# Optimization experiments

Hardware: AMD Instinct MI355X
Metric: run time of the kernel (lower is better)

## Reference

```python
import jax, jax.numpy as jnp
import numpy as np

N = 4096      # nodes = mi_num + dis_num
IN = 4096     # in_size = mi_num + dis_num
H = 1024      # hidd_list = [H, H]
P = 256       # num_proj_hidden
TAU = 0.5
ALPHA = 0.8


def setup_inputs() -> dict:
    key = jax.random.key(0)
    ks = jax.random.split(key, 24)
    u = lambda k, shape, s: jax.random.uniform(k, shape, jnp.float32, -s, s)
    sH = 1.0 / np.sqrt(H)      # HGNN_conv stdv = 1/sqrt(out_ft)
    sP2 = 1.0 / np.sqrt(2 * P)
    sP = 1.0 / np.sqrt(P)
    inp = {
        "x1": jax.random.normal(ks[0], (N, IN), jnp.float32),
        "adj1": jax.random.uniform(ks[1], (N, N), jnp.float32) / N,  # normalized dense hypergraph Laplacian
        "x2": jax.random.normal(ks[2], (N, IN), jnp.float32),
        "adj2": jax.random.uniform(ks[3], (N, N), jnp.float32) / N,
        # hgcn1 (view 1) layers
        "W1a": u(ks[4], (IN, H), sH), "b1a": u(ks[5], (H,), sH),
        "W1b": u(ks[6], (H, H), sH),  "b1b": u(ks[7], (H,), sH),
        # hgcn2 (view 2) layers
        "W2a": u(ks[8], (IN, H), sH), "b2a": u(ks[9], (H,), sH),
        "W2b": u(ks[10], (H, H), sH), "b2b": u(ks[11], (H,), sH),
        # shared projection head (Linear stored as [in, out])
        "fc1_w": u(ks[12], (2 * H, H), sH),     "fc1_b": u(ks[13], (H,), sH),
        "fc11_w": u(ks[14], (H, 2 * P), sP2),   "fc11_b": u(ks[15], (2 * P,), sP2),
        "fc12_w": u(ks[16], (2 * P, P), sP),    "fc12_b": u(ks[17], (P,), sP),
        "fc2_w": u(ks[18], (P, 2 * P), sP2),    "fc2_b": u(ks[19], (2 * P,), sP2),
        "fc3_w": u(ks[20], (2 * P, P), sP),     "fc3_b": u(ks[21], (P,), sP),
    }
    return inp


def _hgcn(x, G, Wa, ba, Wb, bb):
    # HGNN_conv: G @ (x @ W + b), then leaky_relu(0.25); JumpingKnowledge 'cat'
    h1 = jax.nn.leaky_relu(G @ (x @ Wa + ba), 0.25)   # [N, H]
    h2 = jax.nn.leaky_relu(G @ (h1 @ Wb + bb), 0.25)  # [N, H]
    return jnp.concatenate([h1, h2], axis=1)          # [N, 2H]


def _projection(z, fc1_w, fc1_b, fc11_w, fc11_b, fc12_w, fc12_b, fc2_w, fc2_b, fc3_w, fc3_b):
    e = jax.nn.elu
    z = e(z @ fc1_w + fc1_b)
    z = e(z @ fc11_w + fc11_b)
    z = e(z @ fc12_w + fc12_b)
    z = e(z @ fc2_w + fc2_b)
    return z @ fc3_w + fc3_b  # [N, P]


def _sim(z1, z2):
    # InfoNCE-style loss; F.normalize with eps 1e-12
    n1 = z1 / jnp.maximum(jnp.linalg.norm(z1, axis=1, keepdims=True), 1e-12)
    n2 = z2 / jnp.maximum(jnp.linalg.norm(z2, axis=1, keepdims=True), 1e-12)
    refl = jnp.exp((n1 @ n1.T) / TAU)      # [N, N]
    between = jnp.exp((n1 @ n2.T) / TAU)   # [N, N]
    d_b = jnp.diagonal(between)
    d_r = jnp.diagonal(refl)
    loss = -jnp.log(d_b / (refl.sum(1) + between.sum(1) - d_r))
    # torch: loss.sum(dim=-1).mean() on a 1-D vector == scalar sum
    return loss.sum()


def reference(x1, adj1, x2, adj2,
              W1a, b1a, W1b, b1b, W2a, b2a, W2b, b2b,
              fc1_w, fc1_b, fc11_w, fc11_b, fc12_w, fc12_b,
              fc2_w, fc2_b, fc3_w, fc3_b):
    z1 = _hgcn(x1, adj1, W1a, b1a, W1b, b1b)
    z2 = _hgcn(x2, adj2, W2a, b2a, W2b, b2b)
    proj = lambda z: _projection(z, fc1_w, fc1_b, fc11_w, fc11_b, fc12_w, fc12_b, fc2_w, fc2_b, fc3_w, fc3_b)
    h1 = proj(z1)
    h2 = proj(z2)
    loss = ALPHA * _sim(h1, h2) + (1.0 - ALPHA) * _sim(h2, h1)
    return (z1, z2, loss)
```

## Files before the change

kernel.cpp:

```cpp
#include <hip/hip_runtime.h>
#include <hip/hip_bf16.h>
#include <cstdint>

using bf16 = __hip_bfloat16;
typedef __attribute__((ext_vector_type(8))) short short8;
typedef __attribute__((ext_vector_type(4))) short short4v;
typedef __attribute__((ext_vector_type(4))) float floatx4;

#define DEVINL __device__ __forceinline__

DEVINL short bfbits(float v) { return __builtin_bit_cast(short, __float2bfloat16(v)); }

DEVINL void gload_lds16(const void* g, void* l) {
  __builtin_amdgcn_global_load_lds((const __attribute__((address_space(1))) void*)g,
                                   (__attribute__((address_space(3))) void*)l, 16, 0, 0);
}

template<int ACT> DEVINL float activate(float v) {
  if constexpr (ACT == 1) return v > 0.f ? v : 0.25f * v;
  else if constexpr (ACT == 2) return v > 0.f ? v : __expf(v) - 1.f;
  else return v;
}


template<int ACT, int TRANS, int BIAS, int AF32, int OF32, int DUAL>
__global__ __launch_bounds__(256, 2)
void gemm_bt(const void* __restrict__ A1, const void* __restrict__ A2, int lda,
             const bf16* __restrict__ B1, const bf16* __restrict__ B2, int ldb,
             const float* __restrict__ bias1, const float* __restrict__ bias2,
             void* __restrict__ out1, void* __restrict__ out2,
             bf16* __restrict__ outB1, bf16* __restrict__ outB2,
             int ldo, int K)
{
  const int gx = gridDim.x, gy = gridDim.y;
  const int nwg = gx * gy * gridDim.z;
  int bx, by, vz;
  if (nwg & 7) {
    bx = blockIdx.x; by = blockIdx.y; vz = blockIdx.z;
  } else {
    const int flat = blockIdx.x + gx * (blockIdx.y + gy * blockIdx.z);
    const int cpx = nwg >> 3;
    const int w = (flat & 7) * cpx + (flat >> 3);
    bx = w % gx;
    const int tmp = w / gx;
    by = tmp % gy;
    vz = tmp / gy;
  }

  const void* A = vz ? A2 : A1;
  const bf16* B = vz ? B2 : B1;
  const float* bias = vz ? bias2 : bias1;
  void* out = vz ? out2 : out1;
  bf16* outB = vz ? outB2 : outB1;

  constexpr int NBUF = AF32 ? 1 : 2;
  __shared__ bf16 At[NBUF][128 * 64];
  __shared__ bf16 Bt[NBUF][128 * 64];
  const int t = threadIdx.x;
  const int wave = t >> 6, lane = t & 63;
  const int mBase = by * 128, nBase = bx * 128;
  const int wm = (wave >> 1) * 64, wn = (wave & 1) * 64;
  const int q = lane >> 4, lm = lane & 15;
  const int rm = lm & 7;

  floatx4 acc[4][4];
#pragma unroll
  for (int i = 0; i < 4; i++)
#pragma unroll
    for (int j = 0; j < 4; j++) acc[i][j] = (floatx4){0.f, 0.f, 0.f, 0.f};

  if constexpr (!AF32) {
    auto STAGE = [&](int buf, int kb) {
#pragma unroll
      for (int i = 0; i < 4; i++) {
        const int c0 = i * 256 + wave * 64;
        const int c = c0 + lane;
        const int row = c >> 3;
        const int ls = (c & 7) ^ (row & 7);
        const bf16* ga = (const bf16*)A + (size_t)(mBase + row) * lda + kb + (ls << 3);
        const bf16* gb = B + (size_t)(nBase + row) * ldb + kb + (ls << 3);
        gload_lds16(ga, &At[buf][c0 * 8]);
        gload_lds16(gb, &Bt[buf][c0 * 8]);
      }
    };
    int cur = 0;
    STAGE(0, 0);
    for (int kb = 0; kb < K; kb += 64) {
      __syncthreads();
      if (kb + 64 < K) STAGE(cur ^ 1, kb + 64);
#pragma unroll
      for (int ks = 0; ks < 64; ks += 32) {
        const int sl = (ks >> 3) + q;
        short8 af[4], bfr[4];
#pragma unroll
        for (int i = 0; i < 4; i++)
          af[i] = *(const short8*)&At[cur][(wm + i * 16 + lm) * 64 + ((sl ^ rm) << 3)];
#pragma unroll
        for (int j = 0; j < 4; j++)
          bfr[j] = *(const short8*)&Bt[cur][(wn + j * 16 + lm) * 64 + ((sl ^ rm) << 3)];
#pragma unroll
        for (int i = 0; i < 4; i++)
#pragma unroll
          for (int j = 0; j < 4; j++)
            acc[i][j] = __builtin_amdgcn_mfma_f32_16x16x32_bf16(af[i], bfr[j], acc[i][j], 0, 0, 0);
      }
      cur ^= 1;
    }
  } else {
    floatx4 apl[4], aph[4];
    short8 bpb[4];
    auto LA = [&](int kb) {
#pragma unroll
      for (int i = 0; i < 4; i++) {
        int c = i * 256 + t;
        size_t off = (size_t)(mBase + (c >> 3)) * lda + kb + ((c & 7) << 3);
        const float* f = (const float*)A + off;
        apl[i] = *(const floatx4*)f;
        aph[i] = *(const floatx4*)(f + 4);
      }
    };
    auto LB = [&](int kb) {
#pragma unroll
      for (int i = 0; i < 4; i++) {
        int c = i * 256 + t;
        bpb[i] = *(const short8*)(B + (size_t)(nBase + (c >> 3)) * ldb + kb + ((c & 7) << 3));
      }
    };
    LA(0); LB(0);
    for (int kb = 0; kb < K; kb += 64) {
      __syncthreads();
#pragma unroll
      for (int i = 0; i < 4; i++) {
        int c = i * 256 + t;
        const int row = c >> 3;
        const int ps = (c & 7) ^ (row & 7);
        short8 r;
#pragma unroll
        for (int j = 0; j < 4; j++) { r[j] = bfbits(apl[i][j]); r[4 + j] = bfbits(aph[i][j]); }
        *(short8*)&At[0][row * 64 + (ps << 3)] = r;
        *(short8*)&Bt[0][row * 64 + (ps << 3)] = bpb[i];
      }
      __syncthreads();
      if (kb + 64 < K) { LA(kb + 64); LB(kb + 64); }
#pragma unroll
      for (int ks = 0; ks < 64; ks += 32) {
        const int sl = (ks >> 3) + q;
        short8 af[4], bfr[4];
#pragma unroll
        for (int i = 0; i < 4; i++)
          af[i] = *(const short8*)&At[0][(wm + i * 16 + lm) * 64 + ((sl ^ rm) << 3)];
#pragma unroll
        for (int j = 0; j < 4; j++)
          bfr[j] = *(const short8*)&Bt[0][(wn + j * 16 + lm) * 64 + ((sl ^ rm) << 3)];
#pragma unroll
        for (int i = 0; i < 4; i++)
#pragma unroll
          for (int j = 0; j < 4; j++)
            acc[i][j] = __builtin_amdgcn_mfma_f32_16x16x32_bf16(af[i], bfr[j], acc[i][j], 0, 0, 0);
      }
    }
  }

#pragma unroll
  for (int i = 0; i < 4; i++) {
#pragma unroll
    for (int j = 0; j < 4; j++) {
      const int col = nBase + wn + j * 16 + lm;
      float bv2 = 0.f;
      if constexpr (BIAS) bv2 = bias[col];
      if constexpr (TRANS) {
        short4v pk;
#pragma unroll
        for (int r = 0; r < 4; r++)
          pk[r] = bfbits(activate<ACT>(acc[i][j][r] + bv2));
        const int row = mBase + wm + i * 16 + q * 4;
        *(short4v*)&((bf16*)out)[(size_t)col * ldo + row] = pk;
      } else {
#pragma unroll
        for (int r = 0; r < 4; r++) {
          const int row = mBase + wm + i * 16 + q * 4 + r;
          float v = activate<ACT>(acc[i][j][r] + bv2);
          if constexpr (OF32) ((float*)out)[(size_t)row * ldo + col] = v;
          else ((bf16*)out)[(size_t)row * ldo + col] = __float2bfloat16(v);
          if constexpr (DUAL) outB[(size_t)row * ldo + col] = __float2bfloat16(v);
        }
      }
    }
  }
}

__global__ __launch_bounds__(256, 2)
void sim3(const bf16* __restrict__ n1, const bf16* __restrict__ n2,
          float* __restrict__ R11, float* __restrict__ R22,
          float* __restrict__ R12, float* __restrict__ C12)
{
  const bf16 *A, *B; float *Rs, *Cs;
  if (blockIdx.z == 0)      { A = n1; B = n1; Rs = R11; Cs = nullptr; }
  else if (blockIdx.z == 1) { A = n2; B = n2; Rs = R22; Cs = nullptr; }
  else                      { A = n1; B = n2; Rs = R12; Cs = C12; }

  __shared__ bf16 At[128 * 64];
  __shared__ bf16 Bt[128 * 64];
  const int t = threadIdx.x;
  const int wave = t >> 6, lane = t & 63;
  const int mBase = blockIdx.y * 128, nBase = blockIdx.x * 128;
  const int wm = (wave >> 1) * 64, wn = (wave & 1) * 64;
  const int q = lane >> 4, lm = lane & 15;
  const int rm = lm & 7;

  floatx4 acc[4][4];
#pragma unroll
  for (int i = 0; i < 4; i++)
#pragma unroll
    for (int j = 0; j < 4; j++) acc[i][j] = (floatx4){0.f, 0.f, 0.f, 0.f};

  short8 apb[4], bpb[4];
  auto LD = [&](int kb) {
#pragma unroll
    for (int i = 0; i < 4; i++) {
      int c = i * 256 + t;
      apb[i] = *(const short8*)(A + (size_t)(mBase + (c >> 3)) * 256 + kb + ((c & 7) << 3));
      bpb[i] = *(const short8*)(B + (size_t)(nBase + (c >> 3)) * 256 + kb + ((c & 7) << 3));
    }
  };

  LD(0);
  for (int kb = 0; kb < 256; kb += 64) {
    __syncthreads();
#pragma unroll
    for (int i = 0; i < 4; i++) {
      int c = i * 256 + t;
      const int row = c >> 3;
      const int ps = (c & 7) ^ (row & 7);
      *(short8*)&At[row * 64 + (ps << 3)] = apb[i];
      *(short8*)&Bt[row * 64 + (ps << 3)] = bpb[i];
    }
    __syncthreads();
    if (kb + 64 < 256) LD(kb + 64);
#pragma unroll
    for (int ks = 0; ks < 64; ks += 32) {
      const int sl = (ks >> 3) + q;
      short8 af[4], bfr[4];
#pragma unroll
      for (int i = 0; i < 4; i++)
        af[i] = *(const short8*)&At[(wm + i * 16 + lm) * 64 + ((sl ^ rm) << 3)];
#pragma unroll
      for (int j = 0; j < 4; j++)
        bfr[j] = *(const short8*)&Bt[(wn + j * 16 + lm) * 64 + ((sl ^ rm) << 3)];
#pragma unroll
      for (int i = 0; i < 4; i++)
#pragma unroll
        for (int j = 0; j < 4; j++)
          acc[i][j] = __builtin_amdgcn_mfma_f32_16x16x32_bf16(af[i], bfr[j], acc[i][j], 0, 0, 0);
    }
  }

  float rs[4][4], cs[4];
#pragma unroll
  for (int i = 0; i < 4; i++) { cs[i] = 0.f;
#pragma unroll
    for (int r = 0; r < 4; r++) rs[i][r] = 0.f; }

#pragma unroll
  for (int i = 0; i < 4; i++)
#pragma unroll
    for (int j = 0; j < 4; j++)
#pragma unroll
      for (int r = 0; r < 4; r++) {
        float e = __expf(2.f * acc[i][j][r]);
        rs[i][r] += e;
        cs[j] += e;
      }

#pragma unroll
  for (int i = 0; i < 4; i++)
#pragma unroll
    for (int r = 0; r < 4; r++) {
      float v = rs[i][r];
      v += __shfl_xor(v, 1); v += __shfl_xor(v, 2);
      v += __shfl_xor(v, 4); v += __shfl_xor(v, 8);
      if (lm == 0) atomicAdd(&Rs[mBase + wm + i * 16 + q * 4 + r], v);
    }
  if (Cs) {
#pragma unroll
    for (int j = 0; j < 4; j++) {
      float v = cs[j];
      v += __shfl_xor(v, 16); v += __shfl_xor(v, 32);
      if (lane < 16) atomicAdd(&Cs[nBase + wn + j * 16 + lane], v);
    }
  }
}

__global__ void transpose2_f32_bf16(const float* __restrict__ in1, const float* __restrict__ in2,
                                    bf16* __restrict__ out1, bf16* __restrict__ out2, int R, int C)
{
  const float* in = blockIdx.z ? in2 : in1;
  bf16* out = blockIdx.z ? out2 : out1;
  __shared__ float tile[32][33];
  const int bx = blockIdx.x * 32;
  const int by = blockIdx.y * 32;
  const int tx = threadIdx.x & 31, ty = threadIdx.x >> 5;
#pragma unroll
  for (int s = 0; s < 4; s++) {
    int r = ty + s * 8;
    tile[r][tx] = in[(size_t)(by + r) * C + bx + tx];
  }
  __syncthreads();
#pragma unroll
  for (int s = 0; s < 4; s++) {
    int r = ty + s * 8;
    out[(size_t)(bx + r) * R + by + tx] = __float2bfloat16(tile[tx][r]);
  }
}

__global__ void convert2_f32_bf16(const float* __restrict__ in1, const float* __restrict__ in2,
                                  bf16* __restrict__ out1, bf16* __restrict__ out2, int n8)
{
  const float* in = blockIdx.z ? in2 : in1;
  bf16* out = blockIdx.z ? out2 : out1;
  const int i = blockIdx.x * 256 + threadIdx.x;
  if (i >= n8) return;
  const size_t off = (size_t)i * 8;
  floatx4 a = *(const floatx4*)(in + off);
  floatx4 b = *(const floatx4*)(in + off + 4);
  short8 r;
#pragma unroll
  for (int j = 0; j < 4; j++) { r[j] = bfbits(a[j]); r[4 + j] = bfbits(b[j]); }
  *(short8*)(out + off) = r;
}

__global__ void zero_f32(float* __restrict__ p, int n)
{
  int i = blockIdx.x * blockDim.x + threadIdx.x;
  if (i < n) p[i] = 0.f;
}

__global__ void norm_rows2(const bf16* __restrict__ h1, const bf16* __restrict__ h2,
                           bf16* __restrict__ o1, bf16* __restrict__ o2)
{
  const bf16* h = blockIdx.z ? h2 : h1;
  bf16* o = blockIdx.z ? o2 : o1;
  const int row = blockIdx.x * 4 + (threadIdx.x >> 6);
  const int lane = threadIdx.x & 63;
  float v[4]; float ss = 0.f;
#pragma unroll
  for (int j = 0; j < 4; j++) {
    v[j] = __bfloat162float(h[(size_t)row * 256 + lane * 4 + j]);
    ss += v[j] * v[j];
  }
  for (int m = 1; m < 64; m <<= 1) ss += __shfl_xor(ss, m);
  const float s = 1.0f / fmaxf(sqrtf(ss), 1e-12f);
#pragma unroll
  for (int j = 0; j < 4; j++)
    o[(size_t)row * 256 + lane * 4 + j] = __float2bfloat16(v[j] * s);
}

__global__ void loss_partial(const bf16* __restrict__ n1, const bf16* __restrict__ n2,
                             const float* __restrict__ R11, const float* __restrict__ R12,
                             const float* __restrict__ R22, const float* __restrict__ C12,
                             float* __restrict__ lossAcc)
{
  const int row = blockIdx.x * 4 + (threadIdx.x >> 6);
  const int lane = threadIdx.x & 63;
  float d12 = 0.f, d11 = 0.f, d22 = 0.f;
#pragma unroll
  for (int j = 0; j < 4; j++) {
    float a = __bfloat162float(n1[(size_t)row * 256 + lane * 4 + j]);
    float b = __bfloat162float(n2[(size_t)row * 256 + lane * 4 + j]);
    d12 += a * b; d11 += a * a; d22 += b * b;
  }
  for (int m = 1; m < 64; m <<= 1) {
    d12 += __shfl_xor(d12, m); d11 += __shfl_xor(d11, m); d22 += __shfl_xor(d22, m);
  }
  if (lane == 0) {
    float a1 = fmaxf(R11[row] + R12[row] - __expf(2.f * d11), 1e-20f);
    float a2 = fmaxf(R22[row] + C12[row] - __expf(2.f * d22), 1e-20f);
    float l1 = logf(a1) - 2.f * d12;
    float l2 = logf(a2) - 2.f * d12;
    atomicAdd(lossAcc, 0.8f * l1 + 0.2f * l2);
  }
}

__global__ void finalize_loss(const float* __restrict__ lossAcc, float* __restrict__ out)
{
  if (threadIdx.x == 0) out[0] = *lossAcc;
}

extern "C" void kernel_launch(void* const* d_in, const int* in_sizes, int n_in,
                              void* d_out, int out_size, void* d_ws, size_t ws_size,
                              hipStream_t stream)
{
  (void)in_sizes; (void)n_in; (void)out_size;
  const float* x1   = (const float*)d_in[0];
  const float* adj1 = (const float*)d_in[1];
  const float* x2   = (const float*)d_in[2];
  const float* adj2 = (const float*)d_in[3];
  const float* W1a  = (const float*)d_in[4];  const float* b1a = (const float*)d_in[5];
  const float* W1b  = (const float*)d_in[6];  const float* b1b = (const float*)d_in[7];
  const float* W2a  = (const float*)d_in[8];  const float* b2a = (const float*)d_in[9];
  const float* W2b  = (const float*)d_in[10]; const float* b2b = (const float*)d_in[11];
  const float* fc1w = (const float*)d_in[12]; const float* fc1b = (const float*)d_in[13];
  const float* fc11w= (const float*)d_in[14]; const float* fc11b= (const float*)d_in[15];
  const float* fc12w= (const float*)d_in[16]; const float* fc12b= (const float*)d_in[17];
  const float* fc2w = (const float*)d_in[18]; const float* fc2b = (const float*)d_in[19];
  const float* fc3w = (const float*)d_in[20]; const float* fc3b = (const float*)d_in[21];

  float* z1 = (float*)d_out;
  float* z2 = z1 + (size_t)4096 * 2048;
  float* lossOut = z1 + (size_t)2 * 4096 * 2048;

  const size_t MB = 1u << 20;
  char* w = (char*)d_ws;
  bf16* WT1  = (bf16*)(w);
  bf16* WT2  = (bf16*)(w + 8 * MB);
  bf16* TT1  = (bf16*)(w + 16 * MB);
  bf16* TT2  = (bf16*)(w + 24 * MB);
  bf16* zB1  = (bf16*)(w + 32 * MB);
  bf16* zB2  = (bf16*)(w + 48 * MB);
  bf16* fc1T = (bf16*)(w + 64 * MB);
  bf16* fc11T= (bf16*)(w + 68 * MB);
  bf16* fc12T= (bf16*)(w + 69 * MB);
  bf16* fc2T = (bf16*)(w + 69 * MB + 256 * 1024);
  bf16* fc3T = (bf16*)(w + 69 * MB + 512 * 1024);
  float* R11 = (float*)(w + 69 * MB + 768 * 1024);
  float* R12 = R11 + 4096;
  float* R22 = R12 + 4096;
  float* C12 = R22 + 4096;
  float* lossAcc = C12 + 4096;
  bf16* P1_1 = (bf16*)(w);
  bf16* P1_2 = (bf16*)(w + 8 * MB);
  bf16* P2_1 = (bf16*)(w + 16 * MB);
  bf16* P2_2 = (bf16*)(w + 20 * MB);
  bf16* P3_1 = (bf16*)(w + 24 * MB);
  bf16* P3_2 = (bf16*)(w + 26 * MB);
  bf16* P4_1 = (bf16*)(w + 28 * MB);
  bf16* P4_2 = (bf16*)(w);
  bf16* Hp1  = (bf16*)(w + 4 * MB);
  bf16* Hp2  = (bf16*)(w + 6 * MB);
  bf16* n1   = (bf16*)(w + 8 * MB);
  bf16* n2   = (bf16*)(w + 10 * MB);
  bf16* adjB1 = (bf16*)(w + 72 * MB);
  bf16* adjB2 = (bf16*)(w + 104 * MB);
  bf16* xB1   = (bf16*)(w + 136 * MB);
  bf16* xB2   = (bf16*)(w + 168 * MB);
  const bool cvtAdj = ws_size >= 136 * MB;
  const bool cvtX   = ws_size >= 200 * MB;

  dim3 blk(256);

  zero_f32<<<dim3(65), blk, 0, stream>>>(R11, 4 * 4096 + 1);

  if (cvtAdj)
    convert2_f32_bf16<<<dim3(8192, 1, 2), blk, 0, stream>>>(adj1, adj2, adjB1, adjB2, 2097152);
  if (cvtX)
    convert2_f32_bf16<<<dim3(8192, 1, 2), blk, 0, stream>>>(x1, x2, xB1, xB2, 2097152);

  transpose2_f32_bf16<<<dim3(32, 64, 1), blk, 0, stream>>>(fc1w, fc1w, fc1T, fc1T, 2048, 1024);
  transpose2_f32_bf16<<<dim3(16, 32, 1), blk, 0, stream>>>(fc11w, fc11w, fc11T, fc11T, 1024, 512);
  transpose2_f32_bf16<<<dim3(8, 16, 1),  blk, 0, stream>>>(fc12w, fc12w, fc12T, fc12T, 512, 256);
  transpose2_f32_bf16<<<dim3(16, 8, 1),  blk, 0, stream>>>(fc2w, fc2w, fc2T, fc2T, 256, 512);
  transpose2_f32_bf16<<<dim3(8, 16, 1),  blk, 0, stream>>>(fc3w, fc3w, fc3T, fc3T, 512, 256);

  transpose2_f32_bf16<<<dim3(32, 128, 2), blk, 0, stream>>>(W1a, W2a, WT1, WT2, 4096, 1024);
  if (cvtX)
    gemm_bt<0, 1, 1, 0, 0, 0><<<dim3(8, 32, 2), blk, 0, stream>>>(
        xB1, xB2, 4096, WT1, WT2, 4096, b1a, b2a, TT1, TT2, nullptr, nullptr, 4096, 4096);
  else
    gemm_bt<0, 1, 1, 1, 0, 0><<<dim3(8, 32, 2), blk, 0, stream>>>(
        x1, x2, 4096, WT1, WT2, 4096, b1a, b2a, TT1, TT2, nullptr, nullptr, 4096, 4096);
  if (cvtAdj)
    gemm_bt<1, 0, 0, 0, 1, 1><<<dim3(8, 32, 2), blk, 0, stream>>>(
        adjB1, adjB2, 4096, TT1, TT2, 4096, nullptr, nullptr, z1, z2, zB1, zB2, 2048, 4096);
  else
    gemm_bt<1, 0, 0, 1, 1, 1><<<dim3(8, 32, 2), blk, 0, stream>>>(
        adj1, adj2, 4096, TT1, TT2, 4096, nullptr, nullptr, z1, z2, zB1, zB2, 2048, 4096);
  transpose2_f32_bf16<<<dim3(32, 32, 2), blk, 0, stream>>>(W1b, W2b, WT1, WT2, 1024, 1024);
  gemm_bt<0, 1, 1, 0, 0, 0><<<dim3(8, 32, 2), blk, 0, stream>>>(
      zB1, zB2, 2048, WT1, WT2, 1024, b1b, b2b, TT1, TT2, nullptr, nullptr, 4096, 1024);
  if (cvtAdj)
    gemm_bt<1, 0, 0, 0, 1, 1><<<dim3(8, 32, 2), blk, 0, stream>>>(
        adjB1, adjB2, 4096, TT1, TT2, 4096, nullptr, nullptr, z1 + 1024, z2 + 1024, zB1 + 1024, zB2 + 1024, 2048, 4096);
  else
    gemm_bt<1, 0, 0, 1, 1, 1><<<dim3(8, 32, 2), blk, 0, stream>>>(
        adj1, adj2, 4096, TT1, TT2, 4096, nullptr, nullptr, z1 + 1024, z2 + 1024, zB1 + 1024, zB2 + 1024, 2048, 4096);

  gemm_bt<2, 0, 1, 0, 0, 0><<<dim3(8, 32, 2), blk, 0, stream>>>(
      zB1, zB2, 2048, fc1T, fc1T, 2048, fc1b, fc1b, P1_1, P1_2, nullptr, nullptr, 1024, 2048);
  gemm_bt<2, 0, 1, 0, 0, 0><<<dim3(4, 32, 2), blk, 0, stream>>>(
      P1_1, P1_2, 1024, fc11T, fc11T, 1024, fc11b, fc11b, P2_1, P2_2, nullptr, nullptr, 512, 1024);
  gemm_bt<2, 0, 1, 0, 0, 0><<<dim3(2, 32, 2), blk, 0, stream>>>(
      P2_1, P2_2, 512, fc12T, fc12T, 512, fc12b, fc12b, P3_1, P3_2, nullptr, nullptr, 256, 512);
  gemm_bt<2, 0, 1, 0, 0, 0><<<dim3(4, 32, 2), blk, 0, stream>>>(
      P3_1, P3_2, 256, fc2T, fc2T, 256, fc2b, fc2b, P4_1, P4_2, nullptr, nullptr, 512, 256);
  gemm_bt<0, 0, 1, 0, 0, 0><<<dim3(2, 32, 2), blk, 0, stream>>>(
      P4_1, P4_2, 512, fc3T, fc3T, 512, fc3b, fc3b, Hp1, Hp2, nullptr, nullptr, 256, 512);
  norm_rows2<<<dim3(1024, 1, 2), blk, 0, stream>>>(Hp1, Hp2, n1, n2);

  sim3<<<dim3(32, 32, 3), blk, 0, stream>>>(n1, n2, R11, R22, R12, C12);

  loss_partial<<<dim3(1024), blk, 0, stream>>>(n1, n2, R11, R12, R22, C12, lossAcc);
  finalize_loss<<<dim3(1), dim3(64), 0, stream>>>(lossAcc, lossOut);
}
```

Measured before the change: 830.9 us.

## Load B operand fragments directly from global into registers, drop B LDS tile

B tiles are no longer staged through shared memory. Each wave loads its own B MFMA fragments straight from global memory into registers, software-pipelined across the two k-substeps. Dropping the B LDS buffer halves shared memory use, and the launch bound rises to 3 blocks per SM. The tile swizzle order is also flipped so that row tiles vary fastest. This trades LDS traffic and syncs for redundant, less-coalesced global loads of B: each B fragment is read by the two waves that share wn.

```diff
diff --git a/kernel.cpp b/kernel.cpp
--- a/kernel.cpp
+++ b/kernel.cpp
@@ -22,9 +22,8 @@
   else return v;
 }
 
-
 template<int ACT, int TRANS, int BIAS, int AF32, int OF32, int DUAL>
-__global__ __launch_bounds__(256, 2)
+__global__ __launch_bounds__(256, 3)
 void gemm_bt(const void* __restrict__ A1, const void* __restrict__ A2, int lda,
              const bf16* __restrict__ B1, const bf16* __restrict__ B2, int ldb,
              const float* __restrict__ bias1, const float* __restrict__ bias2,
@@ -41,10 +40,10 @@
     const int flat = blockIdx.x + gx * (blockIdx.y + gy * blockIdx.z);
     const int cpx = nwg >> 3;
     const int w = (flat & 7) * cpx + (flat >> 3);
-    bx = w % gx;
-    const int tmp = w / gx;
-    by = tmp % gy;
-    vz = tmp / gy;
+    by = w % gy;
+    const int tmp = w / gy;
+    bx = tmp % gx;
+    vz = tmp / gx;
   }
 
   const void* A = vz ? A2 : A1;
@@ -55,7 +54,6 @@
 
   constexpr int NBUF = AF32 ? 1 : 2;
   __shared__ bf16 At[NBUF][128 * 64];
-  __shared__ bf16 Bt[NBUF][128 * 64];
   const int t = threadIdx.x;
   const int wave = t >> 6, lane = t & 63;
   const int mBase = by * 128, nBase = bx * 128;
@@ -69,6 +67,26 @@
 #pragma unroll
     for (int j = 0; j < 4; j++) acc[i][j] = (floatx4){0.f, 0.f, 0.f, 0.f};
 
+  auto LBF = [&](short8 (&dst)[4], int kb, int ks) {
+#pragma unroll
+    for (int j = 0; j < 4; j++)
+      dst[j] = *(const short8*)(B + (size_t)(nBase + wn + j * 16 + lm) * ldb + kb + ks + q * 8);
+  };
+  auto LDA = [&](short8 (&af)[4], int buf, int sl) {
+#pragma unroll
+    for (int i = 0; i < 4; i++)
+      af[i] = *(const short8*)&At[buf][(wm + i * 16 + lm) * 64 + (((sl + q) ^ rm) << 3)];
+  };
+  auto MM = [&](short8 (&af)[4], short8 (&b)[4]) {
+#pragma unroll
+    for (int i = 0; i < 4; i++)
+#pragma unroll
+      for (int j = 0; j < 4; j++)
+        acc[i][j] = __builtin_amdgcn_mfma_f32_16x16x32_bf16(af[i], b[j], acc[i][j], 0, 0, 0);
+  };
+
+  short8 bC[4], bN[4];
+
   if constexpr (!AF32) {
     auto STAGE = [&](int buf, int kb) {
 #pragma unroll
@@ -78,37 +96,28 @@
         const int row = c >> 3;
         const int ls = (c & 7) ^ (row & 7);
         const bf16* ga = (const bf16*)A + (size_t)(mBase + row) * lda + kb + (ls << 3);
-        const bf16* gb = B + (size_t)(nBase + row) * ldb + kb + (ls << 3);
         gload_lds16(ga, &At[buf][c0 * 8]);
-        gload_lds16(gb, &Bt[buf][c0 * 8]);
       }
     };
     int cur = 0;
     STAGE(0, 0);
+    LBF(bC, 0, 0);
     for (int kb = 0; kb < K; kb += 64) {
       __syncthreads();
-      if (kb + 64 < K) STAGE(cur ^ 1, kb + 64);
-#pragma unroll
-      for (int ks = 0; ks < 64; ks += 32) {
-        const int sl = (ks >> 3) + q;
-        short8 af[4], bfr[4];
-#pragma unroll
-        for (int i = 0; i < 4; i++)
-          af[i] = *(const short8*)&At[cur][(wm + i * 16 + lm) * 64 + ((sl ^ rm) << 3)];
-#pragma unroll
-        for (int j = 0; j < 4; j++)
-          bfr[j] = *(const short8*)&Bt[cur][(wn + j * 16 + lm) * 64 + ((sl ^ rm) << 3)];
-#pragma unroll
-        for (int i = 0; i < 4; i++)
-#pragma unroll
-          for (int j = 0; j < 4; j++)
-            acc[i][j] = __builtin_amdgcn_mfma_f32_16x16x32_bf16(af[i], bfr[j], acc[i][j], 0, 0, 0);
-      }
+      const bool more = (kb + 64 < K);
+      if (more) STAGE(cur ^ 1, kb + 64);
+      LBF(bN, kb, 32);
+      short8 af[4];
+      LDA(af, cur, 0);
+      MM(af, bC);
+      if (more) LBF(bC, kb + 64, 0);
+      short8 ag[4];
+      LDA(ag, cur, 4);
+      MM(ag, bN);
       cur ^= 1;
     }
   } else {
     floatx4 apl[4], aph[4];
-    short8 bpb[4];
     auto LA = [&](int kb) {
 #pragma unroll
       for (int i = 0; i < 4; i++) {
@@ -119,14 +128,8 @@
         aph[i] = *(const floatx4*)(f + 4);
       }
     };
-    auto LB = [&](int kb) {
-#pragma unroll
-      for (int i = 0; i < 4; i++) {
-        int c = i * 256 + t;
-        bpb[i] = *(const short8*)(B + (size_t)(nBase + (c >> 3)) * ldb + kb + ((c & 7) << 3));
-      }
-    };
-    LA(0); LB(0);
+    LA(0);
+    LBF(bC, 0, 0);
     for (int kb = 0; kb < K; kb += 64) {
       __syncthreads();
 #pragma unroll
@@ -138,26 +141,18 @@
 #pragma unroll
         for (int j = 0; j < 4; j++) { r[j] = bfbits(apl[i][j]); r[4 + j] = bfbits(aph[i][j]); }
         *(short8*)&At[0][row * 64 + (ps << 3)] = r;
-        *(short8*)&Bt[0][row * 64 + (ps << 3)] = bpb[i];
       }
       __syncthreads();
-      if (kb + 64 < K) { LA(kb + 64); LB(kb + 64); }
-#pragma unroll
-      for (int ks = 0; ks < 64; ks += 32) {
-        const int sl = (ks >> 3) + q;
-        short8 af[4], bfr[4];
-#pragma unroll
-        for (int i = 0; i < 4; i++)
-          af[i] = *(const short8*)&At[0][(wm + i * 16 + lm) * 64 + ((sl ^ rm) << 3)];
-#pragma unroll
-        for (int j = 0; j < 4; j++)
-          bfr[j] = *(const short8*)&Bt[0][(wn + j * 16 + lm) * 64 + ((sl ^ rm) << 3)];
-#pragma unroll
-        for (int i = 0; i < 4; i++)
-#pragma unroll
-          for (int j = 0; j < 4; j++)
-            acc[i][j] = __builtin_amdgcn_mfma_f32_16x16x32_bf16(af[i], bfr[j], acc[i][j], 0, 0, 0);
-      }
+      const bool more = (kb + 64 < K);
+      if (more) LA(kb + 64);
+      LBF(bN, kb, 32);
+      short8 af[4];
+      LDA(af, 0, 0);
+      MM(af, bC);
+      if (more) LBF(bC, kb + 64, 0);
+      short8 ag[4];
+      LDA(ag, 0, 4);
+      MM(ag, bN);
     }
   }
 
```

Result: slower. 1.071 ms (+28.8%).

## Shrink GEMM tile to 128x64 and load sim3 operands directly from global

Applied to the files above, without the earlier changes.

The generic GEMM tile goes from 128x128 to 128x64, with half-size B staging and a 4x2 accumulator per wave. Launch bounds rise to 3 blocks per SM and every grid's x dimension is doubled to match. The sim3 kernel drops its LDS staging and reads MFMA fragments straight from global memory, relying on cache for the small K=256 operands. Smaller tiles raise occupancy and parallelism but cut arithmetic intensity per loaded byte, and the uncoalesced direct global fragment loads in sim3 may cost bandwidth.

```diff
diff --git a/kernel.cpp b/kernel.cpp
--- a/kernel.cpp
+++ b/kernel.cpp
@@ -22,9 +22,8 @@
   else return v;
 }
 
-
 template<int ACT, int TRANS, int BIAS, int AF32, int OF32, int DUAL>
-__global__ __launch_bounds__(256, 2)
+__global__ __launch_bounds__(256, 3)
 void gemm_bt(const void* __restrict__ A1, const void* __restrict__ A2, int lda,
              const bf16* __restrict__ B1, const bf16* __restrict__ B2, int ldb,
              const float* __restrict__ bias1, const float* __restrict__ bias2,
@@ -55,19 +54,37 @@
 
   constexpr int NBUF = AF32 ? 1 : 2;
   __shared__ bf16 At[NBUF][128 * 64];
-  __shared__ bf16 Bt[NBUF][128 * 64];
+  __shared__ bf16 Bt[NBUF][64 * 64];
   const int t = threadIdx.x;
   const int wave = t >> 6, lane = t & 63;
-  const int mBase = by * 128, nBase = bx * 128;
-  const int wm = (wave >> 1) * 64, wn = (wave & 1) * 64;
+  const int mBase = by * 128, nBase = bx * 64;
+  const int wm = (wave >> 1) * 64, wn = (wave & 1) * 32;
   const int q = lane >> 4, lm = lane & 15;
   const int rm = lm & 7;
 
-  floatx4 acc[4][4];
+  floatx4 acc[4][2];
 #pragma unroll
   for (int i = 0; i < 4; i++)
 #pragma unroll
-    for (int j = 0; j < 4; j++) acc[i][j] = (floatx4){0.f, 0.f, 0.f, 0.f};
+    for (int j = 0; j < 2; j++) acc[i][j] = (floatx4){0.f, 0.f, 0.f, 0.f};
+
+  auto LDA = [&](short8 (&af)[4], int buf, int sl) {
+#pragma unroll
+    for (int i = 0; i < 4; i++)
+      af[i] = *(const short8*)&At[buf][(wm + i * 16 + lm) * 64 + (((sl + q) ^ rm) << 3)];
+  };
+  auto LDB = [&](short8 (&bfr)[2], int buf, int sl) {
+#pragma unroll
+    for (int j = 0; j < 2; j++)
+      bfr[j] = *(const short8*)&Bt[buf][(wn + j * 16 + lm) * 64 + (((sl + q) ^ rm) << 3)];
+  };
+  auto MM = [&](short8 (&af)[4], short8 (&bfr)[2]) {
+#pragma unroll
+    for (int i = 0; i < 4; i++)
+#pragma unroll
+      for (int j = 0; j < 2; j++)
+        acc[i][j] = __builtin_amdgcn_mfma_f32_16x16x32_bf16(af[i], bfr[j], acc[i][j], 0, 0, 0);
+  };
 
   if constexpr (!AF32) {
     auto STAGE = [&](int buf, int kb) {
@@ -77,10 +94,17 @@
         const int c = c0 + lane;
         const int row = c >> 3;
         const int ls = (c & 7) ^ (row & 7);
-        const bf16* ga = (const bf16*)A + (size_t)(mBase + row) * lda + kb + (ls << 3);
-        const bf16* gb = B + (size_t)(nBase + row) * ldb + kb + (ls << 3);
-        gload_lds16(ga, &At[buf][c0 * 8]);
-        gload_lds16(gb, &Bt[buf][c0 * 8]);
+        gload_lds16((const bf16*)A + (size_t)(mBase + row) * lda + kb + (ls << 3),
+                    &At[buf][c0 * 8]);
+      }
+#pragma unroll
+      for (int i = 0; i < 2; i++) {
+        const int c0 = i * 256 + wave * 64;
+        const int c = c0 + lane;
+        const int row = c >> 3;
+        const int ls = (c & 7) ^ (row & 7);
+        gload_lds16(B + (size_t)(nBase + row) * ldb + kb + (ls << 3),
+                    &Bt[buf][c0 * 8]);
       }
     };
     int cur = 0;
@@ -88,40 +112,28 @@
     for (int kb = 0; kb < K; kb += 64) {
       __syncthreads();
       if (kb + 64 < K) STAGE(cur ^ 1, kb + 64);
-#pragma unroll
-      for (int ks = 0; ks < 64; ks += 32) {
-        const int sl = (ks >> 3) + q;
-        short8 af[4], bfr[4];
-#pragma unroll
-        for (int i = 0; i < 4; i++)
-          af[i] = *(const short8*)&At[cur][(wm + i * 16 + lm) * 64 + ((sl ^ rm) << 3)];
-#pragma unroll
-        for (int j = 0; j < 4; j++)
-          bfr[j] = *(const short8*)&Bt[cur][(wn + j * 16 + lm) * 64 + ((sl ^ rm) << 3)];
-#pragma unroll
-        for (int i = 0; i < 4; i++)
-#pragma unroll
-          for (int j = 0; j < 4; j++)
-            acc[i][j] = __builtin_amdgcn_mfma_f32_16x16x32_bf16(af[i], bfr[j], acc[i][j], 0, 0, 0);
-      }
+      short8 af[4], bfr[2];
+      LDA(af, cur, 0); LDB(bfr, cur, 0);
+      MM(af, bfr);
+      LDA(af, cur, 4); LDB(bfr, cur, 4);
+      MM(af, bfr);
       cur ^= 1;
     }
   } else {
     floatx4 apl[4], aph[4];
-    short8 bpb[4];
+    short8 bpb[2];
     auto LA = [&](int kb) {
 #pragma unroll
       for (int i = 0; i < 4; i++) {
         int c = i * 256 + t;
-        size_t off = (size_t)(mBase + (c >> 3)) * lda + kb + ((c & 7) << 3);
-        const float* f = (const float*)A + off;
+        const float* f = (const float*)A + (size_t)(mBase + (c >> 3)) * lda + kb + ((c & 7) << 3);
         apl[i] = *(const floatx4*)f;
         aph[i] = *(const floatx4*)(f + 4);
       }
     };
     auto LB = [&](int kb) {
 #pragma unroll
-      for (int i = 0; i < 4; i++) {
+      for (int i = 0; i < 2; i++) {
         int c = i * 256 + t;
         bpb[i] = *(const short8*)(B + (size_t)(nBase + (c >> 3)) * ldb + kb + ((c & 7) << 3));
       }
@@ -138,33 +150,28 @@
 #pragma unroll
         for (int j = 0; j < 4; j++) { r[j] = bfbits(apl[i][j]); r[4 + j] = bfbits(aph[i][j]); }
         *(short8*)&At[0][row * 64 + (ps << 3)] = r;
+      }
+#pragma unroll
+      for (int i = 0; i < 2; i++) {
+        int c = i * 256 + t;
+        const int row = c >> 3;
+        const int ps = (c & 7) ^ (row & 7);
         *(short8*)&Bt[0][row * 64 + (ps << 3)] = bpb[i];
       }
       __syncthreads();
       if (kb + 64 < K) { LA(kb + 64); LB(kb + 64); }
-#pragma unroll
-      for (int ks = 0; ks < 64; ks += 32) {
-        const int sl = (ks >> 3) + q;
-        short8 af[4], bfr[4];
-#pragma unroll
-        for (int i = 0; i < 4; i++)
-          af[i] = *(const short8*)&At[0][(wm + i * 16 + lm) * 64 + ((sl ^ rm) << 3)];
-#pragma unroll
-        for (int j = 0; j < 4; j++)
-          bfr[j] = *(const short8*)&Bt[0][(wn + j * 16 + lm) * 64 + ((sl ^ rm) << 3)];
-#pragma unroll
-        for (int i = 0; i < 4; i++)
-#pragma unroll
-          for (int j = 0; j < 4; j++)
-            acc[i][j] = __builtin_amdgcn_mfma_f32_16x16x32_bf16(af[i], bfr[j], acc[i][j], 0, 0, 0);
-      }
+      short8 af[4], bfr[2];
+      LDA(af, 0, 0); LDB(bfr, 0, 0);
+      MM(af, bfr);
+      LDA(af, 0, 4); LDB(bfr, 0, 4);
+      MM(af, bfr);
     }
   }
 
 #pragma unroll
   for (int i = 0; i < 4; i++) {
 #pragma unroll
-    for (int j = 0; j < 4; j++) {
+    for (int j = 0; j < 2; j++) {
       const int col = nBase + wn + j * 16 + lm;
       float bv2 = 0.f;
       if constexpr (BIAS) bv2 = bias[col];
@@ -189,7 +196,7 @@
   }
 }
 
-__global__ __launch_bounds__(256, 2)
+__global__ __launch_bounds__(256, 3)
 void sim3(const bf16* __restrict__ n1, const bf16* __restrict__ n2,
           float* __restrict__ R11, float* __restrict__ R22,
           float* __restrict__ R12, float* __restrict__ C12)
@@ -199,14 +206,11 @@
   else if (blockIdx.z == 1) { A = n2; B = n2; Rs = R22; Cs = nullptr; }
   else                      { A = n1; B = n2; Rs = R12; Cs = C12; }
 
-  __shared__ bf16 At[128 * 64];
-  __shared__ bf16 Bt[128 * 64];
   const int t = threadIdx.x;
   const int wave = t >> 6, lane = t & 63;
   const int mBase = blockIdx.y * 128, nBase = blockIdx.x * 128;
   const int wm = (wave >> 1) * 64, wn = (wave & 1) * 64;
   const int q = lane >> 4, lm = lane & 15;
-  const int rm = lm & 7;
 
   floatx4 acc[4][4];
 #pragma unroll
@@ -214,45 +218,20 @@
 #pragma unroll
     for (int j = 0; j < 4; j++) acc[i][j] = (floatx4){0.f, 0.f, 0.f, 0.f};
 
-  short8 apb[4], bpb[4];
-  auto LD = [&](int kb) {
-#pragma unroll
-    for (int i = 0; i < 4; i++) {
-      int c = i * 256 + t;
-      apb[i] = *(const short8*)(A + (size_t)(mBase + (c >> 3)) * 256 + kb + ((c & 7) << 3));
-      bpb[i] = *(const short8*)(B + (size_t)(nBase + (c >> 3)) * 256 + kb + ((c & 7) << 3));
-    }
-  };
-
-  LD(0);
-  for (int kb = 0; kb < 256; kb += 64) {
-    __syncthreads();
-#pragma unroll
-    for (int i = 0; i < 4; i++) {
-      int c = i * 256 + t;
-      const int row = c >> 3;
-      const int ps = (c & 7) ^ (row & 7);
-      *(short8*)&At[row * 64 + (ps << 3)] = apb[i];
-      *(short8*)&Bt[row * 64 + (ps << 3)] = bpb[i];
-    }
-    __syncthreads();
-    if (kb + 64 < 256) LD(kb + 64);
-#pragma unroll
-    for (int ks = 0; ks < 64; ks += 32) {
-      const int sl = (ks >> 3) + q;
-      short8 af[4], bfr[4];
-#pragma unroll
-      for (int i = 0; i < 4; i++)
-        af[i] = *(const short8*)&At[(wm + i * 16 + lm) * 64 + ((sl ^ rm) << 3)];
+#pragma unroll
+  for (int kb = 0; kb < 256; kb += 32) {
+    short8 af[4], bfr[4];
+#pragma unroll
+    for (int i = 0; i < 4; i++)
+      af[i] = *(const short8*)(A + (size_t)(mBase + wm + i * 16 + lm) * 256 + kb + q * 8);
+#pragma unroll
+    for (int j = 0; j < 4; j++)
+      bfr[j] = *(const short8*)(B + (size_t)(nBase + wn + j * 16 + lm) * 256 + kb + q * 8);
+#pragma unroll
+    for (int i = 0; i < 4; i++)
 #pragma unroll
       for (int j = 0; j < 4; j++)
-        bfr[j] = *(const short8*)&Bt[(wn + j * 16 + lm) * 64 + ((sl ^ rm) << 3)];
-#pragma unroll
-      for (int i = 0; i < 4; i++)
-#pragma unroll
-        for (int j = 0; j < 4; j++)
-          acc[i][j] = __builtin_amdgcn_mfma_f32_16x16x32_bf16(af[i], bfr[j], acc[i][j], 0, 0, 0);
-    }
+        acc[i][j] = __builtin_amdgcn_mfma_f32_16x16x32_bf16(af[i], bfr[j], acc[i][j], 0, 0, 0);
   }
 
   float rs[4][4], cs[4];
@@ -463,36 +442,36 @@
 
   transpose2_f32_bf16<<<dim3(32, 128, 2), blk, 0, stream>>>(W1a, W2a, WT1, WT2, 4096, 1024);
   if (cvtX)
-    gemm_bt<0, 1, 1, 0, 0, 0><<<dim3(8, 32, 2), blk, 0, stream>>>(
+    gemm_bt<0, 1, 1, 0, 0, 0><<<dim3(16, 32, 2), blk, 0, stream>>>(
         xB1, xB2, 4096, WT1, WT2, 4096, b1a, b2a, TT1, TT2, nullptr, nullptr, 4096, 4096);
   else
-    gemm_bt<0, 1, 1, 1, 0, 0><<<dim3(8, 32, 2), blk, 0, stream>>>(
+    gemm_bt<0, 1, 1, 1, 0, 0><<<dim3(16, 32, 2), blk, 0, stream>>>(
         x1, x2, 4096, WT1, WT2, 4096, b1a, b2a, TT1, TT2, nullptr, nullptr, 4096, 4096);
   if (cvtAdj)
-    gemm_bt<1, 0, 0, 0, 1, 1><<<dim3(8, 32, 2), blk, 0, stream>>>(
+    gemm_bt<1, 0, 0, 0, 1, 1><<<dim3(16, 32, 2), blk, 0, stream>>>(
         adjB1, adjB2, 4096, TT1, TT2, 4096, nullptr, nullptr, z1, z2, zB1, zB2, 2048, 4096);
   else
-    gemm_bt<1, 0, 0, 1, 1, 1><<<dim3(8, 32, 2), blk, 0, stream>>>(
+    gemm_bt<1, 0, 0, 1, 1, 1><<<dim3(16, 32, 2), blk, 0, stream>>>(
         adj1, adj2, 4096, TT1, TT2, 4096, nullptr, nullptr, z1, z2, zB1, zB2, 2048, 4096);
   transpose2_f32_bf16<<<dim3(32, 32, 2), blk, 0, stream>>>(W1b, W2b, WT1, WT2, 1024, 1024);
-  gemm_bt<0, 1, 1, 0, 0, 0><<<dim3(8, 32, 2), blk, 0, stream>>>(
+  gemm_bt<0, 1, 1, 0, 0, 0><<<dim3(16, 32, 2), blk, 0, stream>>>(
       zB1, zB2, 2048, WT1, WT2, 1024, b1b, b2b, TT1, TT2, nullptr, nullptr, 4096, 1024);
   if (cvtAdj)
-    gemm_bt<1, 0, 0, 0, 1, 1><<<dim3(8, 32, 2), blk, 0, stream>>>(
+    gemm_bt<1, 0, 0, 0, 1, 1><<<dim3(16, 32, 2), blk, 0, stream>>>(
         adjB1, adjB2, 4096, TT1, TT2, 4096, nullptr, nullptr, z1 + 1024, z2 + 1024, zB1 + 1024, zB2 + 1024, 2048, 4096);
   else
-    gemm_bt<1, 0, 0, 1, 1, 1><<<dim3(8, 32, 2), blk, 0, stream>>>(
+    gemm_bt<1, 0, 0, 1, 1, 1><<<dim3(16, 32, 2), blk, 0, stream>>>(
         adj1, adj2, 4096, TT1, TT2, 4096, nullptr, nullptr, z1 + 1024, z2 + 1024, zB1 + 1024, zB2 + 1024, 2048, 4096);
 
+  gemm_bt<2, 0, 1, 0, 0, 0><<<dim3(16, 32, 2), blk, 0, stream>>>(
+      zB1, zB2, 2048, fc1T, fc1T, 2048, fc1b, fc1b, P1_1, P1_2, nullptr, nullptr, 1024, 2048);
   gemm_bt<2, 0, 1, 0, 0, 0><<<dim3(8, 32, 2), blk, 0, stream>>>(
-      zB1, zB2, 2048, fc1T, fc1T, 2048, fc1b, fc1b, P1_1, P1_2, nullptr, nullptr, 1024, 2048);
+      P1_1, P1_2, 1024, fc11T, fc11T, 1024, fc11b, fc11b, P2_1, P2_2, nullptr, nullptr, 512, 1024);
   gemm_bt<2, 0, 1, 0, 0, 0><<<dim3(4, 32, 2), blk, 0, stream>>>(
-      P1_1, P1_2, 1024, fc11T, fc11T, 1024, fc11b, fc11b, P2_1, P2_2, nullptr, nullptr, 512, 1024);
-  gemm_bt<2, 0, 1, 0, 0, 0><<<dim3(2, 32, 2), blk, 0, stream>>>(
       P2_1, P2_2, 512, fc12T, fc12T, 512, fc12b, fc12b, P3_1, P3_2, nullptr, nullptr, 256, 512);
-  gemm_bt<2, 0, 1, 0, 0, 0><<<dim3(4, 32, 2), blk, 0, stream>>>(
+  gemm_bt<2, 0, 1, 0, 0, 0><<<dim3(8, 32, 2), blk, 0, stream>>>(
       P3_1, P3_2, 256, fc2T, fc2T, 256, fc2b, fc2b, P4_1, P4_2, nullptr, nullptr, 512, 256);
-  gemm_bt<0, 0, 1, 0, 0, 0><<<dim3(2, 32, 2), blk, 0, stream>>>(
+  gemm_bt<0, 0, 1, 0, 0, 0><<<dim3(4, 32, 2), blk, 0, stream>>>(
       P4_1, P4_2, 512, fc3T, fc3T, 512, fc3b, fc3b, Hp1, Hp2, nullptr, nullptr, 256, 512);
   norm_rows2<<<dim3(1024, 1, 2), blk, 0, stream>>>(Hp1, Hp2, n1, n2);
 
```

Result: slower. 1.032 ms (+24.2%).
